# Kernel tuning notes

Measured on AMD Instinct MI355X. Metric: run time of the kernel, lower is better.

## Reference

```python
import jax, jax.numpy as jnp
import numpy as np

N, M, H = 200000, 400000, 128
EPS = 1e-12  # torch F.normalize eps


def _l2norm(x):
    # F.normalize(x, p=2, dim=-1): x / max(||x||, eps)
    n = jnp.linalg.norm(x, axis=-1, keepdims=True)
    return x / jnp.maximum(n, EPS)


def message_norm(feat, msg, scale):
    # DGL MessageNorm(learn_scale=True): normalize(msg) * ||feat|| * scale
    feat_norm = jnp.linalg.norm(feat, axis=-1, keepdims=True)
    return _l2norm(msg) * feat_norm * scale


def setup_inputs() -> dict:
    key = jax.random.key(0)
    ks = jax.random.split(key, 8)
    h_src = jax.random.normal(ks[0], (M, H), dtype=jnp.float32)
    c_src = jax.random.normal(ks[1], (M, H), dtype=jnp.float32)
    iou = jax.random.normal(ks[2], (N, 3 * H), dtype=jnp.float32)
    child_idx = jax.random.randint(ks[3], (N, 2), 0, M, dtype=jnp.int64)
    # torch nn.Linear layout: y = x @ W.T + b
    lim_f = 1.0 / np.sqrt(2 * H)
    W_f = jax.random.uniform(ks[4], (2 * H, 2 * H), minval=-lim_f, maxval=lim_f, dtype=jnp.float32)
    b_f = jax.random.uniform(ks[5], (2 * H,), minval=-lim_f, maxval=lim_f, dtype=jnp.float32)
    W_iou = jax.random.uniform(ks[6], (3 * H, 2 * H), minval=-lim_f, maxval=lim_f, dtype=jnp.float32)
    b_iou = jnp.zeros((1, 3 * H), dtype=jnp.float32)
    scale_iou = jnp.ones((), dtype=jnp.float32)
    scale_c = jnp.ones((), dtype=jnp.float32)
    return {"h_src": h_src, "c_src": c_src, "iou": iou, "child_idx": child_idx,
            "W_f": W_f, "b_f": b_f, "W_iou": W_iou, "b_iou": b_iou,
            "scale_iou": scale_iou, "scale_c": scale_c}


def reference(h_src, c_src, iou, child_idx, W_f, b_f, W_iou, b_iou, scale_iou, scale_c):
    # --- reduce_func: gather children, forget gates, weighted cell sum ---
    h_ch = h_src[child_idx]                 # [N, 2, H]
    c_ch = c_src[child_idx]                 # [N, 2, H]
    h_cat = h_ch.reshape(h_ch.shape[0], -1)  # [N, 2H]
    f = jax.nn.sigmoid(h_cat @ W_f.T + b_f).reshape(h_ch.shape)  # [N, 2, H]
    c_sum = jnp.sum(f * c_ch, axis=1)       # [N, H]
    iou_n = message_norm(iou, h_cat, scale_iou) @ W_iou.T  # [N, 3H]
    c_dat = message_norm(c_ch[:, 0, :], c_sum, scale_c)    # [N, H]
    # --- apply_node_func ---
    iou_b = iou_n + b_iou
    i, o, u = jnp.split(iou_b, 3, axis=1)
    c = jax.nn.sigmoid(i) * jnp.tanh(u) + c_dat
    h = jax.nn.sigmoid(o) * jnp.tanh(c)
    return jnp.stack([h, c], axis=1)        # [N, 2, H]
```

## Files before the change

kernel.cpp:

```cpp
#include <hip/hip_runtime.h>
#include <math.h>

typedef __attribute__((ext_vector_type(4))) float f32x4;
typedef __attribute__((ext_vector_type(8))) short bf16x8;
typedef __attribute__((ext_vector_type(4))) short short4v;

#define EPSN 1e-12f
#define TN 32
#define YS 640

__device__ inline short f2bf(float x) {
    union { float f; unsigned u; } v; v.f = x;
    unsigned r = v.u + 0x7fffu + ((v.u >> 16) & 1u);
    return (short)(r >> 16);
}
__device__ inline float bf2f(short s) {
    union { unsigned u; float f; } v;
    v.u = ((unsigned)(unsigned short)s) << 16;
    return v.f;
}
__device__ inline float wsum64(float v) {
#pragma unroll
    for (int m = 32; m > 0; m >>= 1) v += __shfl_xor(v, m);
    return v;
}
__device__ inline float wsum16(float v) {
    v += __shfl_xor(v, 1);
    v += __shfl_xor(v, 2);
    v += __shfl_xor(v, 4);
    v += __shfl_xor(v, 8);
    return v;
}
__device__ inline float sigm(float x) { return 1.0f / (1.0f + __expf(-x)); }
__device__ inline float tanh_fast(float x) {
    float a = fabsf(x);
    float e = __expf(2.0f * a);
    float t = 1.0f - 2.0f / (e + 1.0f);
    return copysignf(t, x);
}

__global__ void prep_B(const float* __restrict__ W_f, const float* __restrict__ W_iou,
                       short* __restrict__ Blin) {
    int t = blockIdx.x * 256 + threadIdx.x;
    if (t >= 8 * 40 * 64) return;
    int lane = t & 63;
    int jb = (t >> 6) % 40;
    int kb = (t >> 6) / 40;
    int j = jb * 16 + (lane & 15);
    int k = kb * 32 + ((lane >> 4) << 3);
    const float* src = (j < 256) ? (W_f + (size_t)j * 256 + k)
                                 : (W_iou + (size_t)(j - 256) * 256 + k);
    bf16x8 v;
#pragma unroll
    for (int e = 0; e < 8; ++e) v[e] = f2bf(src[e]);
    *(bf16x8*)(Blin + (size_t)t * 8) = v;
}

__global__ __launch_bounds__(512, 6) void tree_fused(
    const float* __restrict__ h_src, const float* __restrict__ c_src,
    const float* __restrict__ iou, const int* __restrict__ child_idx,
    const float* __restrict__ b_f, const float* __restrict__ b_iou,
    const float* __restrict__ sc_iou_p, const float* __restrict__ sc_c_p,
    const short* __restrict__ Blin, float* __restrict__ out) {
    __shared__ short U[TN * YS];
    __shared__ float h_n2[TN], iou_n2[TN];
    __shared__ int cc_lds[TN][2];

    const int tid = threadIdx.x;
    const int wave = tid >> 6;
    const int lane = tid & 63;
    const int nbase = blockIdx.x * TN;

    {
        const int child = lane >> 5;
        const int seg = lane & 31;
        int cix[4];
#pragma unroll
        for (int r = 0; r < 4; ++r)
            cix[r] = child_idx[(size_t)(nbase + wave + 8 * r) * 2 + child];
        f32x4 hv[4];
#pragma unroll
        for (int r = 0; r < 4; ++r)
            hv[r] = *(const f32x4*)(h_src + (size_t)cix[r] * 128 + seg * 4);
#pragma unroll
        for (int r = 0; r < 4; ++r) {
            const int nd = wave + 8 * r;
            const int node = nbase + nd;
            short4v a4;
            a4.x = f2bf(hv[r].x); a4.y = f2bf(hv[r].y);
            a4.z = f2bf(hv[r].z); a4.w = f2bf(hv[r].w);
            const int swz = (lane * 8) ^ ((nd & 7) << 4);
            *(short4v*)((char*)U + nd * 512 + swz) = a4;
            if (lane == 0) cc_lds[nd][0] = cix[r];
            if (lane == 32) cc_lds[nd][1] = cix[r];
            float hss = hv[r].x * hv[r].x + hv[r].y * hv[r].y
                      + hv[r].z * hv[r].z + hv[r].w * hv[r].w;
            float iss = 0.f;
#pragma unroll
            for (int q = 0; q < 6; ++q) {
                float v = iou[(size_t)node * 384 + q * 64 + lane];
                iss += v * v;
            }
            hss = wsum64(hss);
            iss = wsum64(iss);
            if (lane == 0) { h_n2[nd] = hss; iou_n2[nd] = iss; }
        }
    }
    __syncthreads();

    f32x4 acc[2][5];
#pragma unroll
    for (int m = 0; m < 2; ++m)
#pragma unroll
        for (int j = 0; j < 5; ++j) acc[m][j] = (f32x4){0.f, 0.f, 0.f, 0.f};

    const int arow = lane & 15;
    const int kgrp = lane >> 4;
#pragma unroll
    for (int kb = 0; kb < 8; ++kb) {
        bf16x8 af[2];
#pragma unroll
        for (int m = 0; m < 2; ++m) {
            const int row = arow + m * 16;
            const int bofs = (kb * 64 + kgrp * 16) ^ ((row & 7) << 4);
            af[m] = *(const bf16x8*)((const char*)U + row * 512 + bofs);
        }
#pragma unroll
        for (int jj = 0; jj < 5; ++jj) {
            const int jb = wave * 5 + jj;
            const bf16x8 bfr = *(const bf16x8*)(Blin + ((size_t)(kb * 40 + jb) * 64 + lane) * 8);
            acc[0][jj] = __builtin_amdgcn_mfma_f32_16x16x32_bf16(af[0], bfr, acc[0][jj], 0, 0, 0);
            acc[1][jj] = __builtin_amdgcn_mfma_f32_16x16x32_bf16(af[1], bfr, acc[1][jj], 0, 0, 0);
        }
    }
    __syncthreads();

#pragma unroll
    for (int m = 0; m < 2; ++m)
#pragma unroll
        for (int jj = 0; jj < 5; ++jj) {
            const int col = (wave * 5 + jj) * 16 + (lane & 15);
            const int r0 = m * 16 + (lane >> 4) * 4;
#pragma unroll
            for (int r = 0; r < 4; ++r) {
                const int row = r0 + r;
                U[row * YS + (col ^ (((row >> 2) & 3) << 4))] = f2bf(acc[m][jj][r]);
            }
        }
    __syncthreads();

    const float sc_iou = sc_iou_p[0];
    const float sc_c = sc_c_p[0];
    const int nd = tid >> 4;
    const int hseg = tid & 15;
    const int h0 = hseg * 8;
    const int node = nbase + nd;

    const int c0i = cc_lds[nd][0];
    const int c1i = cc_lds[nd][1];
    float c0v[8], c1v[8];
    *(f32x4*)&c0v[0] = *(const f32x4*)(c_src + (size_t)c0i * 128 + h0);
    *(f32x4*)&c0v[4] = *(const f32x4*)(c_src + (size_t)c0i * 128 + h0 + 4);
    *(f32x4*)&c1v[0] = *(const f32x4*)(c_src + (size_t)c1i * 128 + h0);
    *(f32x4*)&c1v[4] = *(const f32x4*)(c_src + (size_t)c1i * 128 + h0 + 4);

    float bfv[16];
    *(f32x4*)&bfv[0]  = *(const f32x4*)(b_f + h0);
    *(f32x4*)&bfv[4]  = *(const f32x4*)(b_f + h0 + 4);
    *(f32x4*)&bfv[8]  = *(const f32x4*)(b_f + 128 + h0);
    *(f32x4*)&bfv[12] = *(const f32x4*)(b_f + 128 + h0 + 4);

    const int swz = ((nd >> 2) & 3) << 4;
    const bf16x8 yf0 = *(const bf16x8*)&U[nd * YS + (h0 ^ swz)];
    const bf16x8 yf1 = *(const bf16x8*)&U[nd * YS + ((128 + h0) ^ swz)];
    const bf16x8 yi  = *(const bf16x8*)&U[nd * YS + ((256 + h0) ^ swz)];
    const bf16x8 yo  = *(const bf16x8*)&U[nd * YS + ((384 + h0) ^ swz)];
    const bf16x8 yu  = *(const bf16x8*)&U[nd * YS + ((512 + h0) ^ swz)];

    float c0n2 = 0.f;
#pragma unroll
    for (int e = 0; e < 8; ++e) c0n2 += c0v[e] * c0v[e];
    c0n2 = wsum16(c0n2);

    float cs[8];
    float csn2 = 0.f;
#pragma unroll
    for (int e = 0; e < 8; ++e) {
        const float f0 = sigm(bf2f(yf0[e]) + bfv[e]);
        const float f1 = sigm(bf2f(yf1[e]) + bfv[8 + e]);
        const float v = f0 * c0v[e] + f1 * c1v[e];
        cs[e] = v;
        csn2 += v * v;
    }
    csn2 = wsum16(csn2);

    const float s_iou = sc_iou * sqrtf(iou_n2[nd]) / fmaxf(sqrtf(h_n2[nd]), EPSN);
    const float rs = sc_c * sqrtf(c0n2) / fmaxf(sqrtf(csn2), EPSN);

    float biv[24];
    *(f32x4*)&biv[0]  = *(const f32x4*)(b_iou + h0);
    *(f32x4*)&biv[4]  = *(const f32x4*)(b_iou + h0 + 4);
    *(f32x4*)&biv[8]  = *(const f32x4*)(b_iou + 128 + h0);
    *(f32x4*)&biv[12] = *(const f32x4*)(b_iou + 128 + h0 + 4);
    *(f32x4*)&biv[16] = *(const f32x4*)(b_iou + 256 + h0);
    *(f32x4*)&biv[20] = *(const f32x4*)(b_iou + 256 + h0 + 4);

    f32x4 outh[2], outc[2];
#pragma unroll
    for (int e = 0; e < 8; ++e) {
        const float iv = bf2f(yi[e]) * s_iou + biv[e];
        const float ov = bf2f(yo[e]) * s_iou + biv[8 + e];
        const float uv = bf2f(yu[e]) * s_iou + biv[16 + e];
        const float cval = sigm(iv) * tanh_fast(uv) + cs[e] * rs;
        const float hval = sigm(ov) * tanh_fast(cval);
        ((float*)outh)[e] = hval;
        ((float*)outc)[e] = cval;
    }
    *(f32x4*)(out + (size_t)node * 256 + h0) = outh[0];
    *(f32x4*)(out + (size_t)node * 256 + h0 + 4) = outh[1];
    *(f32x4*)(out + (size_t)node * 256 + 128 + h0) = outc[0];
    *(f32x4*)(out + (size_t)node * 256 + 128 + h0 + 4) = outc[1];
}

extern "C" void kernel_launch(void* const* d_in, const int* in_sizes, int n_in,
                              void* d_out, int out_size, void* d_ws, size_t ws_size,
                              hipStream_t stream) {
    const float* h_src = (const float*)d_in[0];
    const float* c_src = (const float*)d_in[1];
    const float* iou = (const float*)d_in[2];
    const int* cidx = (const int*)d_in[3];
    const float* W_f = (const float*)d_in[4];
    const float* b_f = (const float*)d_in[5];
    const float* W_iou = (const float*)d_in[6];
    const float* b_iou = (const float*)d_in[7];
    const float* s_iou = (const float*)d_in[8];
    const float* s_c = (const float*)d_in[9];
    float* out = (float*)d_out;
    short* Blin = (short*)d_ws;

    const int N = in_sizes[3] / 2;
    hipLaunchKernelGGL(prep_B, dim3(80), dim3(256), 0, stream, W_f, W_iou, Blin);
    hipLaunchKernelGGL(tree_fused, dim3(N / TN), dim3(512), 0, stream,
                       h_src, c_src, iou, cidx, b_f, b_iou, s_iou, s_c, Blin, out);
}
```

Baseline: 275.6 us.

## Halve LDS staging buffer, split epilogue into two passes, fold f-gate bias into accumulators

The GEMM output staging buffer shrinks from 32 to 16 rows, and the epilogue now runs in two passes of 16 nodes each, with 32 threads per node doing 4 elements apiece. Together with a raised launch-bounds occupancy target, the smaller LDS footprint is meant to fit more resident blocks per CU and hide more of the gather latency. The forget-gate bias is preloaded into the MFMA accumulators, b_iou is staged in LDS, and the iou norm loads are vectorized. The cost is an extra pair of barriers per block and tighter register pressure under the new bound.

```diff
diff --git a/kernel.cpp b/kernel.cpp
--- a/kernel.cpp
+++ b/kernel.cpp
@@ -2,6 +2,7 @@
 #include <math.h>
 
 typedef __attribute__((ext_vector_type(4))) float f32x4;
+typedef __attribute__((ext_vector_type(2))) float f32x2;
 typedef __attribute__((ext_vector_type(8))) short bf16x8;
 typedef __attribute__((ext_vector_type(4))) short short4v;
 
@@ -24,11 +25,12 @@
     for (int m = 32; m > 0; m >>= 1) v += __shfl_xor(v, m);
     return v;
 }
-__device__ inline float wsum16(float v) {
+__device__ inline float wsum32(float v) {
     v += __shfl_xor(v, 1);
     v += __shfl_xor(v, 2);
     v += __shfl_xor(v, 4);
     v += __shfl_xor(v, 8);
+    v += __shfl_xor(v, 16);
     return v;
 }
 __device__ inline float sigm(float x) { return 1.0f / (1.0f + __expf(-x)); }
@@ -56,13 +58,14 @@
     *(bf16x8*)(Blin + (size_t)t * 8) = v;
 }
 
-__global__ __launch_bounds__(512, 6) void tree_fused(
+__global__ __launch_bounds__(512, 8) void tree_fused(
     const float* __restrict__ h_src, const float* __restrict__ c_src,
     const float* __restrict__ iou, const int* __restrict__ child_idx,
     const float* __restrict__ b_f, const float* __restrict__ b_iou,
     const float* __restrict__ sc_iou_p, const float* __restrict__ sc_c_p,
     const short* __restrict__ Blin, float* __restrict__ out) {
-    __shared__ short U[TN * YS];
+    __shared__ short U[16 * YS];
+    __shared__ float biou_lds[384];
     __shared__ float h_n2[TN], iou_n2[TN];
     __shared__ int cc_lds[TN][2];
 
@@ -70,6 +73,11 @@
     const int wave = tid >> 6;
     const int lane = tid & 63;
     const int nbase = blockIdx.x * TN;
+
+    const float sc_iou = sc_iou_p[0];
+    const float sc_c = sc_c_p[0];
+
+    if (tid < 384) biou_lds[tid] = b_iou[tid];
 
     {
         const int child = lane >> 5;
@@ -95,12 +103,10 @@
             if (lane == 32) cc_lds[nd][1] = cix[r];
             float hss = hv[r].x * hv[r].x + hv[r].y * hv[r].y
                       + hv[r].z * hv[r].z + hv[r].w * hv[r].w;
-            float iss = 0.f;
-#pragma unroll
-            for (int q = 0; q < 6; ++q) {
-                float v = iou[(size_t)node * 384 + q * 64 + lane];
-                iss += v * v;
-            }
+            const f32x4 v4 = *(const f32x4*)(iou + (size_t)node * 384 + lane * 4);
+            const f32x2 v2 = *(const f32x2*)(iou + (size_t)node * 384 + 256 + lane * 2);
+            float iss = v4.x * v4.x + v4.y * v4.y + v4.z * v4.z + v4.w * v4.w
+                      + v2.x * v2.x + v2.y * v2.y;
             hss = wsum64(hss);
             iss = wsum64(iss);
             if (lane == 0) { h_n2[nd] = hss; iou_n2[nd] = iss; }
@@ -109,11 +115,18 @@
     __syncthreads();
 
     f32x4 acc[2][5];
-#pragma unroll
-    for (int m = 0; m < 2; ++m)
-#pragma unroll
-        for (int j = 0; j < 5; ++j) acc[m][j] = (f32x4){0.f, 0.f, 0.f, 0.f};
-
+    {
+        const int colb = wave * 80 + (lane & 15);
+#pragma unroll
+        for (int jj = 0; jj < 5; ++jj) {
+            const int col = colb + jj * 16;
+            float bv = 0.0f;
+            if (col < 256) bv = b_f[col];
+            const f32x4 a = {bv, bv, bv, bv};
+            acc[0][jj] = a;
+            acc[1][jj] = a;
+        }
+    }
     const int arow = lane & 15;
     const int kgrp = lane >> 4;
 #pragma unroll
@@ -133,93 +146,76 @@
             acc[1][jj] = __builtin_amdgcn_mfma_f32_16x16x32_bf16(af[1], bfr, acc[1][jj], 0, 0, 0);
         }
     }
-    __syncthreads();
-
-#pragma unroll
-    for (int m = 0; m < 2; ++m)
+
+#pragma unroll
+    for (int p = 0; p < 2; ++p) {
+        __syncthreads();
 #pragma unroll
         for (int jj = 0; jj < 5; ++jj) {
-            const int col = (wave * 5 + jj) * 16 + (lane & 15);
-            const int r0 = m * 16 + (lane >> 4) * 4;
+            const int col = wave * 80 + jj * 16 + (lane & 15);
+            const int r0 = (lane >> 4) * 4;
 #pragma unroll
             for (int r = 0; r < 4; ++r) {
                 const int row = r0 + r;
-                U[row * YS + (col ^ (((row >> 2) & 3) << 4))] = f2bf(acc[m][jj][r]);
+                U[row * YS + (col ^ (((row >> 2) & 3) << 4))] = f2bf(acc[p][jj][r]);
             }
         }
-    __syncthreads();
-
-    const float sc_iou = sc_iou_p[0];
-    const float sc_c = sc_c_p[0];
-    const int nd = tid >> 4;
-    const int hseg = tid & 15;
-    const int h0 = hseg * 8;
-    const int node = nbase + nd;
-
-    const int c0i = cc_lds[nd][0];
-    const int c1i = cc_lds[nd][1];
-    float c0v[8], c1v[8];
-    *(f32x4*)&c0v[0] = *(const f32x4*)(c_src + (size_t)c0i * 128 + h0);
-    *(f32x4*)&c0v[4] = *(const f32x4*)(c_src + (size_t)c0i * 128 + h0 + 4);
-    *(f32x4*)&c1v[0] = *(const f32x4*)(c_src + (size_t)c1i * 128 + h0);
-    *(f32x4*)&c1v[4] = *(const f32x4*)(c_src + (size_t)c1i * 128 + h0 + 4);
-
-    float bfv[16];
-    *(f32x4*)&bfv[0]  = *(const f32x4*)(b_f + h0);
-    *(f32x4*)&bfv[4]  = *(const f32x4*)(b_f + h0 + 4);
-    *(f32x4*)&bfv[8]  = *(const f32x4*)(b_f + 128 + h0);
-    *(f32x4*)&bfv[12] = *(const f32x4*)(b_f + 128 + h0 + 4);
-
-    const int swz = ((nd >> 2) & 3) << 4;
-    const bf16x8 yf0 = *(const bf16x8*)&U[nd * YS + (h0 ^ swz)];
-    const bf16x8 yf1 = *(const bf16x8*)&U[nd * YS + ((128 + h0) ^ swz)];
-    const bf16x8 yi  = *(const bf16x8*)&U[nd * YS + ((256 + h0) ^ swz)];
-    const bf16x8 yo  = *(const bf16x8*)&U[nd * YS + ((384 + h0) ^ swz)];
-    const bf16x8 yu  = *(const bf16x8*)&U[nd * YS + ((512 + h0) ^ swz)];
-
-    float c0n2 = 0.f;
-#pragma unroll
-    for (int e = 0; e < 8; ++e) c0n2 += c0v[e] * c0v[e];
-    c0n2 = wsum16(c0n2);
-
-    float cs[8];
-    float csn2 = 0.f;
-#pragma unroll
-    for (int e = 0; e < 8; ++e) {
-        const float f0 = sigm(bf2f(yf0[e]) + bfv[e]);
-        const float f1 = sigm(bf2f(yf1[e]) + bfv[8 + e]);
-        const float v = f0 * c0v[e] + f1 * c1v[e];
-        cs[e] = v;
-        csn2 += v * v;
-    }
-    csn2 = wsum16(csn2);
-
-    const float s_iou = sc_iou * sqrtf(iou_n2[nd]) / fmaxf(sqrtf(h_n2[nd]), EPSN);
-    const float rs = sc_c * sqrtf(c0n2) / fmaxf(sqrtf(csn2), EPSN);
-
-    float biv[24];
-    *(f32x4*)&biv[0]  = *(const f32x4*)(b_iou + h0);
-    *(f32x4*)&biv[4]  = *(const f32x4*)(b_iou + h0 + 4);
-    *(f32x4*)&biv[8]  = *(const f32x4*)(b_iou + 128 + h0);
-    *(f32x4*)&biv[12] = *(const f32x4*)(b_iou + 128 + h0 + 4);
-    *(f32x4*)&biv[16] = *(const f32x4*)(b_iou + 256 + h0);
-    *(f32x4*)&biv[20] = *(const f32x4*)(b_iou + 256 + h0 + 4);
-
-    f32x4 outh[2], outc[2];
-#pragma unroll
-    for (int e = 0; e < 8; ++e) {
-        const float iv = bf2f(yi[e]) * s_iou + biv[e];
-        const float ov = bf2f(yo[e]) * s_iou + biv[8 + e];
-        const float uv = bf2f(yu[e]) * s_iou + biv[16 + e];
-        const float cval = sigm(iv) * tanh_fast(uv) + cs[e] * rs;
-        const float hval = sigm(ov) * tanh_fast(cval);
-        ((float*)outh)[e] = hval;
-        ((float*)outc)[e] = cval;
-    }
-    *(f32x4*)(out + (size_t)node * 256 + h0) = outh[0];
-    *(f32x4*)(out + (size_t)node * 256 + h0 + 4) = outh[1];
-    *(f32x4*)(out + (size_t)node * 256 + 128 + h0) = outc[0];
-    *(f32x4*)(out + (size_t)node * 256 + 128 + h0 + 4) = outc[1];
+        __syncthreads();
+
+        const int ndl = tid >> 5;
+        const int nd = p * 16 + ndl;
+        const int q = tid & 31;
+        const int h0 = q * 4;
+        const int node = nbase + nd;
+
+        const int c0i = cc_lds[nd][0];
+        const int c1i = cc_lds[nd][1];
+        const f32x4 c0v = *(const f32x4*)(c_src + (size_t)c0i * 128 + h0);
+        const f32x4 c1v = *(const f32x4*)(c_src + (size_t)c1i * 128 + h0);
+
+        const int swz = ((ndl >> 2) & 3) << 4;
+        const short4v yf0 = *(const short4v*)&U[ndl * YS + (h0 ^ swz)];
+        const short4v yf1 = *(const short4v*)&U[ndl * YS + ((128 + h0) ^ swz)];
+        const short4v yi  = *(const short4v*)&U[ndl * YS + ((256 + h0) ^ swz)];
+        const short4v yo  = *(const short4v*)&U[ndl * YS + ((384 + h0) ^ swz)];
+        const short4v yu  = *(const short4v*)&U[ndl * YS + ((512 + h0) ^ swz)];
+
+        float c0n2 = c0v.x * c0v.x + c0v.y * c0v.y + c0v.z * c0v.z + c0v.w * c0v.w;
+        c0n2 = wsum32(c0n2);
+
+        float cs[4];
+        float csn2 = 0.f;
+#pragma unroll
+        for (int e = 0; e < 4; ++e) {
+            const float f0 = sigm(bf2f(yf0[e]));
+            const float f1 = sigm(bf2f(yf1[e]));
+            const float v = f0 * ((const float*)&c0v)[e] + f1 * ((const float*)&c1v)[e];
+            cs[e] = v;
+            csn2 += v * v;
+        }
+        csn2 = wsum32(csn2);
+
+        const float s_iou = sc_iou * sqrtf(iou_n2[nd]) / fmaxf(sqrtf(h_n2[nd]), EPSN);
+        const float rs = sc_c * sqrtf(c0n2) / fmaxf(sqrtf(csn2), EPSN);
+
+        const f32x4 bi0 = *(const f32x4*)&biou_lds[h0];
+        const f32x4 bi1 = *(const f32x4*)&biou_lds[128 + h0];
+        const f32x4 bi2 = *(const f32x4*)&biou_lds[256 + h0];
+
+        f32x4 outh, outc;
+#pragma unroll
+        for (int e = 0; e < 4; ++e) {
+            const float iv = bf2f(yi[e]) * s_iou + ((const float*)&bi0)[e];
+            const float ov = bf2f(yo[e]) * s_iou + ((const float*)&bi1)[e];
+            const float uv = bf2f(yu[e]) * s_iou + ((const float*)&bi2)[e];
+            const float cval = sigm(iv) * tanh_fast(uv) + cs[e] * rs;
+            const float hval = sigm(ov) * tanh_fast(cval);
+            ((float*)&outh)[e] = hval;
+            ((float*)&outc)[e] = cval;
+        }
+        *(f32x4*)(out + (size_t)node * 256 + h0) = outh;
+        *(f32x4*)(out + (size_t)node * 256 + 128 + h0) = outc;
+    }
 }
 
 extern "C" void kernel_launch(void* const* d_in, const int* in_sizes, int n_in,
```

After: 379.3 us. +37.7%, slower.

## Split fused GEMM into forget-gate and iou phases to cut LDS and registers

Applied to the files above, without the earlier changes.

The single 640-wide MFMA pass is split into two phases: first the forget-gate columns, with bias folded into the accumulator init, stored to a small LDS region. The cell-sum computation and c_src gather then overlap with the iou GEMM, whose results reuse the A-tile LDS area. LDS drops from 40KB to 32KB and live accumulators from 10 to at most 6 per wave, and launch bounds are raised to 7 blocks per CU for higher occupancy. The iou norm load is also vectorised. It adds one extra barrier, and the forget-gate bias is now added before bf16 rounding rather than after.

```diff
diff --git a/kernel.cpp b/kernel.cpp
--- a/kernel.cpp
+++ b/kernel.cpp
@@ -2,12 +2,12 @@
 #include <math.h>
 
 typedef __attribute__((ext_vector_type(4))) float f32x4;
+typedef __attribute__((ext_vector_type(2))) float f32x2;
 typedef __attribute__((ext_vector_type(8))) short bf16x8;
 typedef __attribute__((ext_vector_type(4))) short short4v;
 
 #define EPSN 1e-12f
 #define TN 32
-#define YS 640
 
 __device__ inline short f2bf(float x) {
     union { float f; unsigned u; } v; v.f = x;
@@ -56,13 +56,13 @@
     *(bf16x8*)(Blin + (size_t)t * 8) = v;
 }
 
-__global__ __launch_bounds__(512, 6) void tree_fused(
+__global__ __launch_bounds__(512, 7) void tree_fused(
     const float* __restrict__ h_src, const float* __restrict__ c_src,
     const float* __restrict__ iou, const int* __restrict__ child_idx,
     const float* __restrict__ b_f, const float* __restrict__ b_iou,
     const float* __restrict__ sc_iou_p, const float* __restrict__ sc_c_p,
     const short* __restrict__ Blin, float* __restrict__ out) {
-    __shared__ short U[TN * YS];
+    __shared__ short U[16384];
     __shared__ float h_n2[TN], iou_n2[TN];
     __shared__ int cc_lds[TN][2];
 
@@ -70,6 +70,9 @@
     const int wave = tid >> 6;
     const int lane = tid & 63;
     const int nbase = blockIdx.x * TN;
+
+    const float sc_iou = sc_iou_p[0];
+    const float sc_c = sc_c_p[0];
 
     {
         const int child = lane >> 5;
@@ -95,12 +98,10 @@
             if (lane == 32) cc_lds[nd][1] = cix[r];
             float hss = hv[r].x * hv[r].x + hv[r].y * hv[r].y
                       + hv[r].z * hv[r].z + hv[r].w * hv[r].w;
-            float iss = 0.f;
-#pragma unroll
-            for (int q = 0; q < 6; ++q) {
-                float v = iou[(size_t)node * 384 + q * 64 + lane];
-                iss += v * v;
-            }
+            const f32x4 v4 = *(const f32x4*)(iou + (size_t)node * 384 + lane * 4);
+            const f32x2 v2 = *(const f32x2*)(iou + (size_t)node * 384 + 256 + lane * 2);
+            float iss = v4.x * v4.x + v4.y * v4.y + v4.z * v4.z + v4.w * v4.w
+                      + v2.x * v2.x + v2.y * v2.y;
             hss = wsum64(hss);
             iss = wsum64(iss);
             if (lane == 0) { h_n2[nd] = hss; iou_n2[nd] = iss; }
@@ -108,14 +109,57 @@
     }
     __syncthreads();
 
-    f32x4 acc[2][5];
-#pragma unroll
-    for (int m = 0; m < 2; ++m)
-#pragma unroll
-        for (int j = 0; j < 5; ++j) acc[m][j] = (f32x4){0.f, 0.f, 0.f, 0.f};
-
     const int arow = lane & 15;
     const int kgrp = lane >> 4;
+    const int nd = tid >> 4;
+    const int h0 = (tid & 15) * 8;
+
+    {
+        f32x4 accf[2][2];
+#pragma unroll
+        for (int jj = 0; jj < 2; ++jj) {
+            const float bv = b_f[(wave * 2 + jj) * 16 + (lane & 15)];
+            const f32x4 a = {bv, bv, bv, bv};
+            accf[0][jj] = a;
+            accf[1][jj] = a;
+        }
+#pragma unroll
+        for (int kb = 0; kb < 8; ++kb) {
+            bf16x8 af[2];
+#pragma unroll
+            for (int m = 0; m < 2; ++m) {
+                const int row = arow + m * 16;
+                const int bofs = (kb * 64 + kgrp * 16) ^ ((row & 7) << 4);
+                af[m] = *(const bf16x8*)((const char*)U + row * 512 + bofs);
+            }
+#pragma unroll
+            for (int jj = 0; jj < 2; ++jj) {
+                const int jbg = wave * 2 + jj;
+                const bf16x8 bfr = *(const bf16x8*)(Blin + ((size_t)(kb * 40 + jbg) * 64 + lane) * 8);
+                accf[0][jj] = __builtin_amdgcn_mfma_f32_16x16x32_bf16(af[0], bfr, accf[0][jj], 0, 0, 0);
+                accf[1][jj] = __builtin_amdgcn_mfma_f32_16x16x32_bf16(af[1], bfr, accf[1][jj], 0, 0, 0);
+            }
+        }
+#pragma unroll
+        for (int m = 0; m < 2; ++m)
+#pragma unroll
+            for (int jj = 0; jj < 2; ++jj) {
+                const int col = (wave * 2 + jj) * 16 + (lane & 15);
+                const int r0 = m * 16 + (lane >> 4) * 4;
+#pragma unroll
+                for (int r = 0; r < 4; ++r) {
+                    const int row = r0 + r;
+                    U[8192 + row * 256 + (col ^ (((row >> 2) & 3) << 4))] = f2bf(accf[m][jj][r]);
+                }
+            }
+    }
+    __syncthreads();
+
+    f32x4 accio[2][3];
+#pragma unroll
+    for (int m = 0; m < 2; ++m)
+#pragma unroll
+        for (int jj = 0; jj < 3; ++jj) accio[m][jj] = (f32x4){0.f, 0.f, 0.f, 0.f};
 #pragma unroll
     for (int kb = 0; kb < 8; ++kb) {
         bf16x8 af[2];
@@ -126,100 +170,98 @@
             af[m] = *(const bf16x8*)((const char*)U + row * 512 + bofs);
         }
 #pragma unroll
-        for (int jj = 0; jj < 5; ++jj) {
-            const int jb = wave * 5 + jj;
-            const bf16x8 bfr = *(const bf16x8*)(Blin + ((size_t)(kb * 40 + jb) * 64 + lane) * 8);
-            acc[0][jj] = __builtin_amdgcn_mfma_f32_16x16x32_bf16(af[0], bfr, acc[0][jj], 0, 0, 0);
-            acc[1][jj] = __builtin_amdgcn_mfma_f32_16x16x32_bf16(af[1], bfr, acc[1][jj], 0, 0, 0);
-        }
+        for (int jj = 0; jj < 3; ++jj) {
+            const int jbg = 16 + wave * 3 + jj;
+            const bf16x8 bfr = *(const bf16x8*)(Blin + ((size_t)(kb * 40 + jbg) * 64 + lane) * 8);
+            accio[0][jj] = __builtin_amdgcn_mfma_f32_16x16x32_bf16(af[0], bfr, accio[0][jj], 0, 0, 0);
+            accio[1][jj] = __builtin_amdgcn_mfma_f32_16x16x32_bf16(af[1], bfr, accio[1][jj], 0, 0, 0);
+        }
+    }
+
+    float csr[8];
+    float s_iou;
+    {
+        const int c0i = cc_lds[nd][0];
+        const int c1i = cc_lds[nd][1];
+        float c0v[8], c1v[8];
+        *(f32x4*)&c0v[0] = *(const f32x4*)(c_src + (size_t)c0i * 128 + h0);
+        *(f32x4*)&c0v[4] = *(const f32x4*)(c_src + (size_t)c0i * 128 + h0 + 4);
+        *(f32x4*)&c1v[0] = *(const f32x4*)(c_src + (size_t)c1i * 128 + h0);
+        *(f32x4*)&c1v[4] = *(const f32x4*)(c_src + (size_t)c1i * 128 + h0 + 4);
+
+        const int fsw = ((nd >> 2) & 3) << 4;
+        const bf16x8 yf0 = *(const bf16x8*)&U[8192 + nd * 256 + (h0 ^ fsw)];
+        const bf16x8 yf1 = *(const bf16x8*)&U[8192 + nd * 256 + ((128 + h0) ^ fsw)];
+
+        float c0n2 = 0.f;
+#pragma unroll
+        for (int e = 0; e < 8; ++e) c0n2 += c0v[e] * c0v[e];
+        c0n2 = wsum16(c0n2);
+
+        float cs[8];
+        float csn2 = 0.f;
+#pragma unroll
+        for (int e = 0; e < 8; ++e) {
+            const float f0 = sigm(bf2f(yf0[e]));
+            const float f1 = sigm(bf2f(yf1[e]));
+            const float v = f0 * c0v[e] + f1 * c1v[e];
+            cs[e] = v;
+            csn2 += v * v;
+        }
+        csn2 = wsum16(csn2);
+
+        const float rs = sc_c * sqrtf(c0n2) / fmaxf(sqrtf(csn2), EPSN);
+#pragma unroll
+        for (int e = 0; e < 8; ++e) csr[e] = cs[e] * rs;
+        s_iou = sc_iou * sqrtf(iou_n2[nd]) / fmaxf(sqrtf(h_n2[nd]), EPSN);
     }
     __syncthreads();
 
 #pragma unroll
     for (int m = 0; m < 2; ++m)
 #pragma unroll
-        for (int jj = 0; jj < 5; ++jj) {
-            const int col = (wave * 5 + jj) * 16 + (lane & 15);
+        for (int jj = 0; jj < 3; ++jj) {
+            const int col = (wave * 3 + jj) * 16 + (lane & 15);
             const int r0 = m * 16 + (lane >> 4) * 4;
 #pragma unroll
             for (int r = 0; r < 4; ++r) {
                 const int row = r0 + r;
-                U[row * YS + (col ^ (((row >> 2) & 3) << 4))] = f2bf(acc[m][jj][r]);
-            }
-        }
-    __syncthreads();
-
-    const float sc_iou = sc_iou_p[0];
-    const float sc_c = sc_c_p[0];
-    const int nd = tid >> 4;
-    const int hseg = tid & 15;
-    const int h0 = hseg * 8;
-    const int node = nbase + nd;
-
-    const int c0i = cc_lds[nd][0];
-    const int c1i = cc_lds[nd][1];
-    float c0v[8], c1v[8];
-    *(f32x4*)&c0v[0] = *(const f32x4*)(c_src + (size_t)c0i * 128 + h0);
-    *(f32x4*)&c0v[4] = *(const f32x4*)(c_src + (size_t)c0i * 128 + h0 + 4);
-    *(f32x4*)&c1v[0] = *(const f32x4*)(c_src + (size_t)c1i * 128 + h0);
-    *(f32x4*)&c1v[4] = *(const f32x4*)(c_src + (size_t)c1i * 128 + h0 + 4);
-
-    float bfv[16];
-    *(f32x4*)&bfv[0]  = *(const f32x4*)(b_f + h0);
-    *(f32x4*)&bfv[4]  = *(const f32x4*)(b_f + h0 + 4);
-    *(f32x4*)&bfv[8]  = *(const f32x4*)(b_f + 128 + h0);
-    *(f32x4*)&bfv[12] = *(const f32x4*)(b_f + 128 + h0 + 4);
-
-    const int swz = ((nd >> 2) & 3) << 4;
-    const bf16x8 yf0 = *(const bf16x8*)&U[nd * YS + (h0 ^ swz)];
-    const bf16x8 yf1 = *(const bf16x8*)&U[nd * YS + ((128 + h0) ^ swz)];
-    const bf16x8 yi  = *(const bf16x8*)&U[nd * YS + ((256 + h0) ^ swz)];
-    const bf16x8 yo  = *(const bf16x8*)&U[nd * YS + ((384 + h0) ^ swz)];
-    const bf16x8 yu  = *(const bf16x8*)&U[nd * YS + ((512 + h0) ^ swz)];
-
-    float c0n2 = 0.f;
-#pragma unroll
-    for (int e = 0; e < 8; ++e) c0n2 += c0v[e] * c0v[e];
-    c0n2 = wsum16(c0n2);
-
-    float cs[8];
-    float csn2 = 0.f;
-#pragma unroll
-    for (int e = 0; e < 8; ++e) {
-        const float f0 = sigm(bf2f(yf0[e]) + bfv[e]);
-        const float f1 = sigm(bf2f(yf1[e]) + bfv[8 + e]);
-        const float v = f0 * c0v[e] + f1 * c1v[e];
-        cs[e] = v;
-        csn2 += v * v;
-    }
-    csn2 = wsum16(csn2);
-
-    const float s_iou = sc_iou * sqrtf(iou_n2[nd]) / fmaxf(sqrtf(h_n2[nd]), EPSN);
-    const float rs = sc_c * sqrtf(c0n2) / fmaxf(sqrtf(csn2), EPSN);
-
-    float biv[24];
-    *(f32x4*)&biv[0]  = *(const f32x4*)(b_iou + h0);
-    *(f32x4*)&biv[4]  = *(const f32x4*)(b_iou + h0 + 4);
-    *(f32x4*)&biv[8]  = *(const f32x4*)(b_iou + 128 + h0);
-    *(f32x4*)&biv[12] = *(const f32x4*)(b_iou + 128 + h0 + 4);
-    *(f32x4*)&biv[16] = *(const f32x4*)(b_iou + 256 + h0);
-    *(f32x4*)&biv[20] = *(const f32x4*)(b_iou + 256 + h0 + 4);
-
-    f32x4 outh[2], outc[2];
-#pragma unroll
-    for (int e = 0; e < 8; ++e) {
-        const float iv = bf2f(yi[e]) * s_iou + biv[e];
-        const float ov = bf2f(yo[e]) * s_iou + biv[8 + e];
-        const float uv = bf2f(yu[e]) * s_iou + biv[16 + e];
-        const float cval = sigm(iv) * tanh_fast(uv) + cs[e] * rs;
-        const float hval = sigm(ov) * tanh_fast(cval);
-        ((float*)outh)[e] = hval;
-        ((float*)outc)[e] = cval;
-    }
-    *(f32x4*)(out + (size_t)node * 256 + h0) = outh[0];
-    *(f32x4*)(out + (size_t)node * 256 + h0 + 4) = outh[1];
-    *(f32x4*)(out + (size_t)node * 256 + 128 + h0) = outc[0];
-    *(f32x4*)(out + (size_t)node * 256 + 128 + h0 + 4) = outc[1];
+                U[row * 384 + (col ^ (((row >> 2) & 3) << 4))] = f2bf(accio[m][jj][r]);
+            }
+        }
+    __syncthreads();
+
+    {
+        const int iosw = ((nd >> 2) & 3) << 4;
+        const bf16x8 yi = *(const bf16x8*)&U[nd * 384 + (h0 ^ iosw)];
+        const bf16x8 yo = *(const bf16x8*)&U[nd * 384 + ((128 + h0) ^ iosw)];
+        const bf16x8 yu = *(const bf16x8*)&U[nd * 384 + ((256 + h0) ^ iosw)];
+
+        float biv[24];
+        *(f32x4*)&biv[0]  = *(const f32x4*)(b_iou + h0);
+        *(f32x4*)&biv[4]  = *(const f32x4*)(b_iou + h0 + 4);
+        *(f32x4*)&biv[8]  = *(const f32x4*)(b_iou + 128 + h0);
+        *(f32x4*)&biv[12] = *(const f32x4*)(b_iou + 128 + h0 + 4);
+        *(f32x4*)&biv[16] = *(const f32x4*)(b_iou + 256 + h0);
+        *(f32x4*)&biv[20] = *(const f32x4*)(b_iou + 256 + h0 + 4);
+
+        const int node = nbase + nd;
+        f32x4 outh[2], outc[2];
+#pragma unroll
+        for (int e = 0; e < 8; ++e) {
+            const float iv = bf2f(yi[e]) * s_iou + biv[e];
+            const float ov = bf2f(yo[e]) * s_iou + biv[8 + e];
+            const float uv = bf2f(yu[e]) * s_iou + biv[16 + e];
+            const float cval = sigm(iv) * tanh_fast(uv) + csr[e];
+            const float hval = sigm(ov) * tanh_fast(cval);
+            ((float*)outh)[e] = hval;
+            ((float*)outc)[e] = cval;
+        }
+        *(f32x4*)(out + (size_t)node * 256 + h0) = outh[0];
+        *(f32x4*)(out + (size_t)node * 256 + h0 + 4) = outh[1];
+        *(f32x4*)(out + (size_t)node * 256 + 128 + h0) = outc[0];
+        *(f32x4*)(out + (size_t)node * 256 + 128 + h0 + 4) = outc[1];
+    }
 }
 
 extern "C" void kernel_launch(void* const* d_in, const int* in_sizes, int n_in,
```

After: 281.0 us. No clear change (+2.0%).
